# Kernel optimization log

Measured on AMD Instinct MI355X. Metric: run time of the kernel, lower is better.

## Reference

```python
import jax, jax.numpy as jnp
import numpy as np

B, S, D, H, E, K = 4, 2048, 1024, 2048, 8, 2


def setup_inputs() -> dict:
    key = jax.random.key(0)
    ks = jax.random.split(key, 5)
    x = jax.random.normal(ks[0], (B, S, D), dtype=jnp.float32)
    Wr = jax.random.normal(ks[1], (D, E), dtype=jnp.float32) * 0.02  # router weight
    w1 = jax.random.normal(ks[2], (E, D, H), dtype=jnp.float32) * 0.02  # gate proj per expert
    w3 = jax.random.normal(ks[3], (E, D, H), dtype=jnp.float32) * 0.02  # up proj per expert
    w2 = jax.random.normal(ks[4], (E, H, D), dtype=jnp.float32) * 0.02  # down proj per expert
    return {"x": x, "Wr": Wr, "w1": w1, "w2": w2, "w3": w3}


def reference(x, Wr, w1, w2, w3):
    b, s, d = x.shape
    e = Wr.shape[1]
    flat = x.reshape(b * s, d)                      # [T, D]
    logits = flat @ Wr                              # [T, E]
    probs = jax.nn.softmax(logits, axis=-1)
    vals, idx = jax.lax.top_k(probs, K)             # [T, K]
    weights = vals / jnp.sum(vals, axis=-1, keepdims=True)
    onehot = jax.nn.one_hot(idx, e, dtype=flat.dtype)   # [T, K, E]
    cw = jnp.einsum('tke,tk->te', onehot, weights)      # combine weight per (token, expert)

    # naive dense: every expert computes every token, masked by combine weights
    out = jnp.zeros_like(flat)
    for ei in range(e):  # fixed small structural loop over experts
        h = jax.nn.silu(flat @ w1[ei]) * (flat @ w3[ei])   # [T, H]
        out = out + (h @ w2[ei]) * cw[:, ei:ei + 1]

    # aux load-balancing loss (usage uses any() over top-k slots, as in torch code)
    usage = (onehot.sum(axis=1) > 0).astype(flat.dtype).mean(axis=0)  # [E]
    prob_mass = probs.mean(axis=0)                                     # [E]
    aux_loss = e * jnp.sum(usage * prob_mass)
    return out.reshape(b, s, d), aux_loss
```

## Files before the change

kernel.cpp:

```cpp
#include <hip/hip_runtime.h>
#include <hip/hip_bf16.h>
#include <cstdint>
#include <cstddef>

#define T_TOK 8192
#define DIM   1024
#define HID   2048
#define NE    8
#define CAP   2816

typedef __attribute__((ext_vector_type(8))) short bf16x8;
typedef __attribute__((ext_vector_type(4))) float f32x4;
using bf16 = __hip_bfloat16;

__device__ __forceinline__ void gload16(const bf16* g, bf16* l) {
    __builtin_amdgcn_global_load_lds(
        (const __attribute__((address_space(1))) unsigned int*)(g),
        (__attribute__((address_space(3))) unsigned int*)(l), 16, 0, 0);
}
__device__ __forceinline__ float b2f(unsigned short u) {
    return __uint_as_float(((unsigned int)u) << 16);
}
#define MFMA16(a, b, c) __builtin_amdgcn_mfma_f32_16x16x32_bf16((a), (b), (c), 0, 0, 0)

__global__ __launch_bounds__(256) void k_transpose_all(const float* __restrict__ w1,
                                                       const float* __restrict__ w3,
                                                       const float* __restrict__ w2,
                                                       bf16* __restrict__ w1t,
                                                       bf16* __restrict__ w3t,
                                                       bf16* __restrict__ w2t) {
    __shared__ float tile[64][65];
    int z = blockIdx.z;
    const float* in = (z == 0) ? w1 : (z == 1) ? w3 : w2;
    bf16* out = (z == 0) ? w1t : (z == 1) ? w3t : w2t;
    int R = (z == 2) ? HID : DIM;
    int C = (z == 2) ? DIM : HID;
    int e = blockIdx.y;
    int ct = C >> 6;
    int r0 = (blockIdx.x / ct) << 6;
    int c0 = (blockIdx.x % ct) << 6;
    const float* src = in + (size_t)e * R * C;
    bf16* dst = out + (size_t)e * R * C;
    int s = threadIdx.x & 15, g = threadIdx.x >> 4;
#pragma unroll
    for (int j = 0; j < 4; ++j) {
        int row = j * 16 + g;
        float4 v = *(const float4*)(src + (size_t)(r0 + row) * C + c0 + s * 4);
        tile[row][s * 4 + 0] = v.x; tile[row][s * 4 + 1] = v.y;
        tile[row][s * 4 + 2] = v.z; tile[row][s * 4 + 3] = v.w;
    }
    __syncthreads();
#pragma unroll
    for (int j = 0; j < 4; ++j) {
        int c = j * 16 + g;
        int r = s * 4;
        bf16 o[4] = {__float2bfloat16(tile[r][c]),     __float2bfloat16(tile[r + 1][c]),
                     __float2bfloat16(tile[r + 2][c]), __float2bfloat16(tile[r + 3][c])};
        *(uint2*)(dst + (size_t)(c0 + c) * R + r0 + r) = *(const uint2*)o;
    }
}

__global__ __launch_bounds__(256) void k_logits(const float* __restrict__ x,
                                                const float* __restrict__ Wr,
                                                float* __restrict__ logits,
                                                bf16* __restrict__ xb) {
    __shared__ float wl[NE][DIM];
    for (int o = threadIdx.x; o < NE * DIM; o += 256) {
        int e = o >> 10, d = o & (DIM - 1);
        wl[e][d] = Wr[d * NE + e];
    }
    __syncthreads();
    int wid = threadIdx.x >> 6, lane = threadIdx.x & 63;
    int t = blockIdx.x * 4 + wid;
    const float* xr = x + (size_t)t * DIM;
    double acc[NE];
#pragma unroll
    for (int e = 0; e < NE; ++e) acc[e] = 0.0;
#pragma unroll
    for (int i = 0; i < DIM / 256; ++i) {
        int base = i * 256 + lane * 4;
        float4 v = *(const float4*)(xr + base);
        bf16 o[4] = {__float2bfloat16(v.x), __float2bfloat16(v.y),
                     __float2bfloat16(v.z), __float2bfloat16(v.w)};
        *(uint2*)(xb + (size_t)t * DIM + base) = *(const uint2*)o;
#pragma unroll
        for (int e = 0; e < NE; ++e)
            acc[e] += (double)v.x * wl[e][base] + (double)v.y * wl[e][base + 1]
                    + (double)v.z * wl[e][base + 2] + (double)v.w * wl[e][base + 3];
    }
#pragma unroll
    for (int e = 0; e < NE; ++e) {
        double v = acc[e];
        for (int m = 32; m >= 1; m >>= 1) v += __shfl_xor(v, m);
        if (lane == 0) logits[t * NE + e] = (float)v;
    }
}

__global__ __launch_bounds__(256) void k_route(const float* __restrict__ logits,
                                               int* counts, int* seg_tok, float* seg_w,
                                               int* slotpos, float* probsum) {
    int t = blockIdx.x * 256 + threadIdx.x;
    float l[NE];
#pragma unroll
    for (int e = 0; e < NE; ++e) l[e] = logits[t * NE + e];
    float mx = l[0];
#pragma unroll
    for (int e = 1; e < NE; ++e) mx = fmaxf(mx, l[e]);
    float p[NE], s = 0.f;
#pragma unroll
    for (int e = 0; e < NE; ++e) { p[e] = expf(l[e] - mx); s += p[e]; }
    float inv = 1.f / s;
#pragma unroll
    for (int e = 0; e < NE; ++e) p[e] *= inv;
    int e0 = 0; float v0 = p[0];
#pragma unroll
    for (int e = 1; e < NE; ++e) if (p[e] > v0) { v0 = p[e]; e0 = e; }
    int e1 = -1; float v1 = -1.f;
#pragma unroll
    for (int e = 0; e < NE; ++e) if (e != e0 && p[e] > v1) { v1 = p[e]; e1 = e; }
    float wsum = v0 + v1;
    float w0 = v0 / wsum, w1 = v1 / wsum;

    int lane = threadIdx.x & 63, wid = threadIdx.x >> 6;
    __shared__ float ps[4][NE];
#pragma unroll
    for (int e = 0; e < NE; ++e) {
        float v = p[e];
        for (int m = 32; m >= 1; m >>= 1) v += __shfl_xor(v, m);
        if (lane == 0) ps[wid][e] = v;
    }
    __syncthreads();
    if (threadIdx.x < NE) {
        float v = ps[0][threadIdx.x] + ps[1][threadIdx.x] + ps[2][threadIdx.x] + ps[3][threadIdx.x];
        atomicAdd(&probsum[threadIdx.x], v);
    }
    for (int slot = 0; slot < 2; ++slot) {
        int   e  = slot ? e1 : e0;
        float wv = slot ? w1 : w0;
#pragma unroll
        for (int ex = 0; ex < NE; ++ex) {
            unsigned long long m = __ballot(e == ex);
            if (e == ex) {
                int leader = __ffsll(m) - 1;
                int base = 0;
                if (lane == leader) base = atomicAdd(&counts[ex], __popcll(m));
                base = __shfl(base, leader);
                int pos = base + (int)__popcll(m & ((1ull << lane) - 1ull));
                if (pos < CAP) {
                    seg_tok[ex * CAP + pos] = t;
                    seg_w[ex * CAP + pos]  = wv;
                    slotpos[2 * t + slot]  = ex * CAP + pos;
                } else {
                    slotpos[2 * t + slot]  = -1;
                }
            }
        }
    }
}

__global__ __launch_bounds__(512, 2) void k_gemm1(const bf16* __restrict__ xb,
                                                  const bf16* __restrict__ w1t,
                                                  const bf16* __restrict__ w3t,
                                                  const int* __restrict__ counts,
                                                  const int* __restrict__ seg_tok,
                                                  bf16* __restrict__ h) {
    __shared__ __align__(16) bf16 lds[24576];
    __shared__ int toks[128];
    const int NTL = HID / 128;
    int flat = blockIdx.y * gridDim.x + blockIdx.x;
    int cpx  = (gridDim.x * NE) >> 3;
    int swz  = (flat & 7) * cpx + (flat >> 3);
    int e    = swz / gridDim.x;
    int tile = swz % gridDim.x;
    int mtile = tile / NTL, ntile = tile % NTL;
    int cnt = counts[e]; if (cnt > CAP) cnt = CAP;
    if (mtile * 128 >= cnt) return;

    int tx = threadIdx.x, lane = tx & 63, w = tx >> 6;
    if (tx < 128) {
        int slot = mtile * 128 + tx;
        toks[tx] = seg_tok[e * CAP + (slot < cnt ? slot : 0)];
    }
    __syncthreads();

    int l8 = lane >> 3;
    int sch = (((lane & 7) ^ l8) << 3);
    const bf16* sp[6];
    bf16* dp[6];
#pragma unroll
    for (int i = 0; i < 6; ++i) {
        int c = w * 6 + i;
        dp[i] = lds + c * 512 + (lane << 3);
        if (c < 16)
            sp[i] = xb + (size_t)toks[c * 8 + l8] * DIM + sch;
        else if (c < 32)
            sp[i] = w1t + ((size_t)e * HID + ntile * 128 + (c - 16) * 8 + l8) * DIM + sch;
        else
            sp[i] = w3t + ((size_t)e * HID + ntile * 128 + (c - 32) * 8 + l8) * DIM + sch;
    }

    int l15 = lane & 15, lh = lane >> 4;
    int role = w >> 2, rh = (w >> 1) & 1, ch = w & 1;
    const int bbase = 8192 + role * 8192;
    f32x4 acc[4][4];
    f32x4 zero4 = {0.f, 0.f, 0.f, 0.f};
#pragma unroll
    for (int m = 0; m < 4; ++m)
#pragma unroll
        for (int n = 0; n < 4; ++n) acc[m][n] = zero4;

    const int NT = DIM / 64;
#pragma unroll 1
    for (int k = 0; k < NT; ++k) {
#pragma unroll
        for (int i = 0; i < 6; ++i) { gload16(sp[i], dp[i]); sp[i] += 64; }
        __syncthreads();
#pragma unroll
        for (int ks = 0; ks < 2; ++ks) {
            int co = ((((ks << 2) | lh) ^ (l15 & 7)) << 3);
            bf16x8 af[4], bb[4];
#pragma unroll
            for (int m = 0; m < 4; ++m)
                af[m] = *(const bf16x8*)(lds + (rh * 64 + m * 16 + l15) * 64 + co);
#pragma unroll
            for (int n = 0; n < 4; ++n)
                bb[n] = *(const bf16x8*)(lds + bbase + (ch * 64 + n * 16 + l15) * 64 + co);
#pragma unroll
            for (int n = 0; n < 4; ++n)
#pragma unroll
                for (int m = 0; m < 4; ++m)
                    acc[m][n] = MFMA16(af[m], bb[n], acc[m][n]);
        }
        __syncthreads();
    }

    if (role == 1) {
#pragma unroll
        for (int m = 0; m < 4; ++m)
#pragma unroll
            for (int n = 0; n < 4; ++n)
#pragma unroll
                for (int r = 0; r < 4; ++r) {
                    int row = rh * 64 + m * 16 + lh * 4 + r;
                    int col = ch * 64 + n * 16 + l15;
                    lds[row * 128 + col] = __float2bfloat16(acc[m][n][r]);
                }
    }
    __syncthreads();
    if (role == 0) {
        bf16* hdst = h + ((size_t)e * CAP + (size_t)mtile * 128) * HID + ntile * 128;
#pragma unroll
        for (int m = 0; m < 4; ++m)
#pragma unroll
            for (int n = 0; n < 4; ++n)
#pragma unroll
                for (int r = 0; r < 4; ++r) {
                    int row = rh * 64 + m * 16 + lh * 4 + r;
                    int col = ch * 64 + n * 16 + l15;
                    float gg = acc[m][n][r];
                    float uu = b2f(*(const unsigned short*)&lds[row * 128 + col]);
                    float hv = gg / (1.f + __expf(-gg)) * uu;
                    hdst[(size_t)row * HID + col] = __float2bfloat16(hv);
                }
    }
}

__global__ __launch_bounds__(256, 3) void k_gemm2(const bf16* __restrict__ hbuf,
                                                  const bf16* __restrict__ w2t,
                                                  const int* __restrict__ counts,
                                                  const float* __restrict__ seg_w,
                                                  bf16* __restrict__ ybuf) {
    __shared__ __align__(16) bf16 lds[16384];
    __shared__ float wts[128];
    const int NTL = DIM / 128;
    int flat = blockIdx.y * gridDim.x + blockIdx.x;
    int cpx  = (gridDim.x * NE) >> 3;
    int swz  = (flat & 7) * cpx + (flat >> 3);
    int e    = swz / gridDim.x;
    int tile = swz % gridDim.x;
    int mtile = tile / NTL, ntile = tile % NTL;
    int cnt = counts[e]; if (cnt > CAP) cnt = CAP;
    if (mtile * 128 >= cnt) return;

    int tx = threadIdx.x, lane = tx & 63, w = tx >> 6;
    if (tx < 128) {
        int slot = mtile * 128 + tx;
        wts[tx] = (slot < cnt) ? seg_w[e * CAP + slot] : 0.f;
    }
    __syncthreads();

    int l8 = lane >> 3;
    int sch = (((lane & 7) ^ l8) << 3);
    const bf16* sA[4];
    const bf16* sB[4];
#pragma unroll
    for (int i = 0; i < 4; ++i) {
        sA[i] = hbuf + ((size_t)e * CAP + mtile * 128 + w * 32 + i * 8 + l8) * HID + sch;
        sB[i] = w2t + ((size_t)e * DIM + ntile * 128 + w * 32 + i * 8 + l8) * HID + sch;
    }
    bf16* dA = lds + w * 2048 + (lane << 3);
    bf16* dB = lds + 8192 + w * 2048 + (lane << 3);

    int l15 = lane & 15, lh = lane >> 4;
    int wm = w >> 1, wn = w & 1;
    f32x4 acc[4][4];
    f32x4 zero4 = {0.f, 0.f, 0.f, 0.f};
#pragma unroll
    for (int m = 0; m < 4; ++m)
#pragma unroll
        for (int n = 0; n < 4; ++n) acc[m][n] = zero4;

    const int NT = HID / 64;
#pragma unroll 1
    for (int k = 0; k < NT; ++k) {
#pragma unroll
        for (int i = 0; i < 4; ++i) {
            gload16(sA[i], dA + i * 512); sA[i] += 64;
            gload16(sB[i], dB + i * 512); sB[i] += 64;
        }
        __syncthreads();
#pragma unroll
        for (int ks = 0; ks < 2; ++ks) {
            int co = ((((ks << 2) | lh) ^ (l15 & 7)) << 3);
            bf16x8 af[4], bf_[4];
#pragma unroll
            for (int m = 0; m < 4; ++m) {
                int row = wm * 64 + m * 16 + l15;
                af[m] = *(const bf16x8*)(lds + row * 64 + co);
                int br = wn * 64 + m * 16 + l15;
                bf_[m] = *(const bf16x8*)(lds + 8192 + br * 64 + co);
            }
#pragma unroll
            for (int n = 0; n < 4; ++n)
#pragma unroll
                for (int m = 0; m < 4; ++m)
                    acc[m][n] = MFMA16(af[m], bf_[n], acc[m][n]);
        }
        __syncthreads();
    }

    bf16* ydst = ybuf + ((size_t)e * CAP + (size_t)mtile * 128) * DIM + ntile * 128;
#pragma unroll
    for (int m = 0; m < 4; ++m)
#pragma unroll
        for (int n = 0; n < 4; ++n)
#pragma unroll
            for (int r = 0; r < 4; ++r) {
                int row = wm * 64 + m * 16 + lh * 4 + r;
                int col = wn * 64 + n * 16 + l15;
                ydst[(size_t)row * DIM + col] = __float2bfloat16(acc[m][n][r] * wts[row]);
            }
}

__global__ __launch_bounds__(256) void k_combine(const bf16* __restrict__ yb,
                                                 const int* __restrict__ slotpos,
                                                 const int* __restrict__ counts,
                                                 const float* __restrict__ probsum,
                                                 float* __restrict__ out) {
#pragma unroll
    for (int j = 0; j < 2; ++j) {
        int t = blockIdx.x * 2 + j;
        int s0 = slotpos[2 * t], s1 = slotpos[2 * t + 1];
        int d = threadIdx.x * 4;
        float4 a = {0.f, 0.f, 0.f, 0.f};
        if (s0 >= 0) {
            ushort4 v = *(const ushort4*)(yb + (size_t)s0 * DIM + d);
            a.x += b2f(v.x); a.y += b2f(v.y); a.z += b2f(v.z); a.w += b2f(v.w);
        }
        if (s1 >= 0) {
            ushort4 v = *(const ushort4*)(yb + (size_t)s1 * DIM + d);
            a.x += b2f(v.x); a.y += b2f(v.y); a.z += b2f(v.z); a.w += b2f(v.w);
        }
        *(float4*)(out + (size_t)t * DIM + d) = a;
    }
    if (blockIdx.x == 0 && threadIdx.x == 0) {
        float s = 0.f;
        for (int e = 0; e < NE; ++e)
            s += ((float)counts[e] / (float)T_TOK) * (probsum[e] / (float)T_TOK);
        out[(size_t)T_TOK * DIM] = (float)NE * s;
    }
}

extern "C" void kernel_launch(void* const* d_in, const int* in_sizes, int n_in,
                              void* d_out, int out_size, void* d_ws, size_t ws_size,
                              hipStream_t stream) {
    const float* x  = (const float*)d_in[0];
    const float* Wr = (const float*)d_in[1];
    const float* w1 = (const float*)d_in[2];
    const float* w2 = (const float*)d_in[3];
    const float* w3 = (const float*)d_in[4];
    float* out = (float*)d_out;

    char* ws = (char*)d_ws;
    size_t off = 0;
    auto alloc = [&](size_t bytes) { void* p = ws + off; off += (bytes + 255) & ~(size_t)255; return p; };
    bf16*  xb      = (bf16*)alloc((size_t)T_TOK * DIM * 2);
    bf16*  w1t     = (bf16*)alloc((size_t)NE * HID * DIM * 2);
    bf16*  w3t     = (bf16*)alloc((size_t)NE * HID * DIM * 2);
    bf16*  w2t     = (bf16*)alloc((size_t)NE * DIM * HID * 2);
    bf16*  hbuf    = (bf16*)alloc((size_t)NE * CAP * HID * 2);
    float* logits  = (float*)alloc((size_t)T_TOK * NE * 4);
    int*   counts  = (int*)alloc(256);
    int*   segtok  = (int*)alloc((size_t)NE * CAP * 4);
    float* segw    = (float*)alloc((size_t)NE * CAP * 4);
    int*   slotpos = (int*)alloc((size_t)T_TOK * 2 * 4);
    float* probsum = (float*)alloc(256);
    bf16*  ybuf    = w1t;
    (void)ws_size; (void)in_sizes; (void)n_in;

    hipMemsetAsync(counts, 0, 256, stream);
    hipMemsetAsync(probsum, 0, 256, stream);

    k_logits<<<T_TOK / 4, 256, 0, stream>>>(x, Wr, logits, xb);
    k_route<<<T_TOK / 256, 256, 0, stream>>>(logits, counts, segtok, segw, slotpos, probsum);

    dim3 gt((DIM / 64) * (HID / 64), NE, 3);
    k_transpose_all<<<gt, 256, 0, stream>>>(w1, w3, w2, w1t, w3t, w2t);

    dim3 g1((CAP / 128) * (HID / 128), NE);
    k_gemm1<<<g1, 512, 0, stream>>>(xb, w1t, w3t, counts, segtok, hbuf);
    dim3 g2((CAP / 128) * (DIM / 128), NE);
    k_gemm2<<<g2, 256, 0, stream>>>(hbuf, w2t, counts, segw, ybuf);

    k_combine<<<T_TOK / 2, 256, 0, stream>>>(ybuf, slotpos, counts, probsum, out);
}
```

Measured before the change: 378.4 us.

## Double-buffer LDS tiles with K=32 steps in both expert GEMM kernels

Both expert GEMM kernels switch from single-buffered 64-wide K tiles to double-buffered 32-wide K tiles. The next tile's global-to-LDS load is issued before computing on the current one, so only one barrier per iteration remains. The LDS layout and swizzle are reworked for the 32-column rows. This aims to overlap memory latency with MFMA work, at the cost of twice as many loop iterations and less compute per barrier.

New measurement: 421.5 us. 11.4% more time.

```diff
diff --git a/kernel.cpp b/kernel.cpp
--- a/kernel.cpp
+++ b/kernel.cpp
@@ -183,25 +183,28 @@
     }
     __syncthreads();
 
-    int l8 = lane >> 3;
-    int sch = (((lane & 7) ^ l8) << 3);
-    const bf16* sp[6];
-    bf16* dp[6];
-#pragma unroll
-    for (int i = 0; i < 6; ++i) {
-        int c = w * 6 + i;
-        dp[i] = lds + c * 512 + (lane << 3);
-        if (c < 16)
-            sp[i] = xb + (size_t)toks[c * 8 + l8] * DIM + sch;
-        else if (c < 32)
-            sp[i] = w1t + ((size_t)e * HID + ntile * 128 + (c - 16) * 8 + l8) * DIM + sch;
+    int lr = lane >> 2;
+    int scol = (((lane & 3) ^ ((lane >> 3) & 3)) << 3);
+    const bf16* sp[3];
+    bf16* dp[3];
+#pragma unroll
+    for (int i = 0; i < 3; ++i) {
+        int c = w * 3 + i;
+        int region = c >> 3, stripe = c & 7;
+        int row = stripe * 16 + lr;
+        dp[i] = lds + region * 4096 + stripe * 512 + (lane << 3);
+        if (region == 0)
+            sp[i] = xb + (size_t)toks[row] * DIM + scol;
+        else if (region == 1)
+            sp[i] = w1t + ((size_t)e * HID + ntile * 128 + row) * DIM + scol;
         else
-            sp[i] = w3t + ((size_t)e * HID + ntile * 128 + (c - 32) * 8 + l8) * DIM + sch;
+            sp[i] = w3t + ((size_t)e * HID + ntile * 128 + row) * DIM + scol;
     }
 
     int l15 = lane & 15, lh = lane >> 4;
     int role = w >> 2, rh = (w >> 1) & 1, ch = w & 1;
-    const int bbase = 8192 + role * 8192;
+    const int bbase = 4096 + role * 4096;
+    const int co = ((lh ^ ((l15 >> 1) & 3)) << 3);
     f32x4 acc[4][4];
     f32x4 zero4 = {0.f, 0.f, 0.f, 0.f};
 #pragma unroll
@@ -209,28 +212,31 @@
 #pragma unroll
         for (int n = 0; n < 4; ++n) acc[m][n] = zero4;
 
-    const int NT = DIM / 64;
+#pragma unroll
+    for (int i = 0; i < 3; ++i) { gload16(sp[i], dp[i]); sp[i] += 32; }
+    __syncthreads();
+
+    const int NT = DIM / 32;
 #pragma unroll 1
     for (int k = 0; k < NT; ++k) {
-#pragma unroll
-        for (int i = 0; i < 6; ++i) { gload16(sp[i], dp[i]); sp[i] += 64; }
-        __syncthreads();
-#pragma unroll
-        for (int ks = 0; ks < 2; ++ks) {
-            int co = ((((ks << 2) | lh) ^ (l15 & 7)) << 3);
-            bf16x8 af[4], bb[4];
+        int sb = (k & 1) * 12288;
+        int nb = ((k + 1) & 1) * 12288;
+        if (k + 1 < NT) {
+#pragma unroll
+            for (int i = 0; i < 3; ++i) { gload16(sp[i], dp[i] + nb); sp[i] += 32; }
+        }
+        bf16x8 af[4], bb[4];
+#pragma unroll
+        for (int m = 0; m < 4; ++m)
+            af[m] = *(const bf16x8*)(lds + sb + (rh * 64 + m * 16 + l15) * 32 + co);
+#pragma unroll
+        for (int n = 0; n < 4; ++n)
+            bb[n] = *(const bf16x8*)(lds + sb + bbase + (ch * 64 + n * 16 + l15) * 32 + co);
+#pragma unroll
+        for (int n = 0; n < 4; ++n)
 #pragma unroll
             for (int m = 0; m < 4; ++m)
-                af[m] = *(const bf16x8*)(lds + (rh * 64 + m * 16 + l15) * 64 + co);
-#pragma unroll
-            for (int n = 0; n < 4; ++n)
-                bb[n] = *(const bf16x8*)(lds + bbase + (ch * 64 + n * 16 + l15) * 64 + co);
-#pragma unroll
-            for (int n = 0; n < 4; ++n)
-#pragma unroll
-                for (int m = 0; m < 4; ++m)
-                    acc[m][n] = MFMA16(af[m], bb[n], acc[m][n]);
-        }
+                acc[m][n] = MFMA16(af[m], bb[n], acc[m][n]);
         __syncthreads();
     }
 
@@ -289,20 +295,25 @@
     }
     __syncthreads();
 
-    int l8 = lane >> 3;
-    int sch = (((lane & 7) ^ l8) << 3);
-    const bf16* sA[4];
-    const bf16* sB[4];
+    int lr = lane >> 2;
+    int scol = (((lane & 3) ^ ((lane >> 3) & 3)) << 3);
+    const bf16* sp[4];
+    bf16* dp[4];
 #pragma unroll
     for (int i = 0; i < 4; ++i) {
-        sA[i] = hbuf + ((size_t)e * CAP + mtile * 128 + w * 32 + i * 8 + l8) * HID + sch;
-        sB[i] = w2t + ((size_t)e * DIM + ntile * 128 + w * 32 + i * 8 + l8) * HID + sch;
-    }
-    bf16* dA = lds + w * 2048 + (lane << 3);
-    bf16* dB = lds + 8192 + w * 2048 + (lane << 3);
+        int c = w * 4 + i;
+        int region = c >> 3, stripe = c & 7;
+        int row = stripe * 16 + lr;
+        dp[i] = lds + region * 4096 + stripe * 512 + (lane << 3);
+        if (region == 0)
+            sp[i] = hbuf + ((size_t)e * CAP + mtile * 128 + row) * HID + scol;
+        else
+            sp[i] = w2t + ((size_t)e * DIM + ntile * 128 + row) * HID + scol;
+    }
 
     int l15 = lane & 15, lh = lane >> 4;
     int wm = w >> 1, wn = w & 1;
+    const int co = ((lh ^ ((l15 >> 1) & 3)) << 3);
     f32x4 acc[4][4];
     f32x4 zero4 = {0.f, 0.f, 0.f, 0.f};
 #pragma unroll
@@ -310,32 +321,30 @@
 #pragma unroll
         for (int n = 0; n < 4; ++n) acc[m][n] = zero4;
 
-    const int NT = HID / 64;
+#pragma unroll
+    for (int i = 0; i < 4; ++i) { gload16(sp[i], dp[i]); sp[i] += 32; }
+    __syncthreads();
+
+    const int NT = HID / 32;
 #pragma unroll 1
     for (int k = 0; k < NT; ++k) {
-#pragma unroll
-        for (int i = 0; i < 4; ++i) {
-            gload16(sA[i], dA + i * 512); sA[i] += 64;
-            gload16(sB[i], dB + i * 512); sB[i] += 64;
-        }
-        __syncthreads();
-#pragma unroll
-        for (int ks = 0; ks < 2; ++ks) {
-            int co = ((((ks << 2) | lh) ^ (l15 & 7)) << 3);
-            bf16x8 af[4], bf_[4];
-#pragma unroll
-            for (int m = 0; m < 4; ++m) {
-                int row = wm * 64 + m * 16 + l15;
-                af[m] = *(const bf16x8*)(lds + row * 64 + co);
-                int br = wn * 64 + m * 16 + l15;
-                bf_[m] = *(const bf16x8*)(lds + 8192 + br * 64 + co);
-            }
-#pragma unroll
-            for (int n = 0; n < 4; ++n)
-#pragma unroll
-                for (int m = 0; m < 4; ++m)
-                    acc[m][n] = MFMA16(af[m], bf_[n], acc[m][n]);
-        }
+        int sb = (k & 1) * 8192;
+        int nb = ((k + 1) & 1) * 8192;
+        if (k + 1 < NT) {
+#pragma unroll
+            for (int i = 0; i < 4; ++i) { gload16(sp[i], dp[i] + nb); sp[i] += 32; }
+        }
+        bf16x8 af[4], bf_[4];
+#pragma unroll
+        for (int m = 0; m < 4; ++m) {
+            af[m]  = *(const bf16x8*)(lds + sb + (wm * 64 + m * 16 + l15) * 32 + co);
+            bf_[m] = *(const bf16x8*)(lds + sb + 4096 + (wn * 64 + m * 16 + l15) * 32 + co);
+        }
+#pragma unroll
+        for (int n = 0; n < 4; ++n)
+#pragma unroll
+            for (int m = 0; m < 4; ++m)
+                acc[m][n] = MFMA16(af[m], bf_[n], acc[m][n]);
         __syncthreads();
     }
 
```
